# Optimization experiments

Hardware: AMD Instinct MI355X
Metric: run time of the kernel (lower is better)

## Reference

```python
import jax, jax.numpy as jnp
import numpy as np

B, H, W, P, KS = 4, 512, 512, 40000, 7
PAD = KS // 2
N = B * P
DIM, DEPTH, HID = 128, 2, 512


def _build_sparse_map():
    rng = np.random.default_rng(0)
    grid = np.full((B, H + 2 * PAD, W + 2 * PAD), N, dtype=np.int64)  # N = missing
    coords = np.empty((N, 3), np.int64)
    for b in range(B):
        flat = rng.choice(H * W, P, replace=False)
        xs, ys = flat // W, flat % W
        idx = np.arange(b * P, (b + 1) * P)
        grid[b, xs + PAD, ys + PAD] = idx
        coords[idx, 0], coords[idx, 1], coords[idx, 2] = b, xs, ys
    nbr = np.empty((N, KS * KS), np.int64)
    k = 0
    for dx in range(-PAD, PAD + 1):
        for dy in range(-PAD, PAD + 1):
            nbr[:, k] = grid[coords[:, 0], coords[:, 1] + PAD + dx, coords[:, 2] + PAD + dy]
            k += 1
    return nbr


def setup_inputs() -> dict:
    key = jax.random.key(0)
    ks = jax.random.split(key, 12)
    s = 0.02
    inp = {
        "feats": jax.random.normal(ks[0], (N, DIM), jnp.float32),
        "w_dw": jax.random.normal(ks[1], (DEPTH, KS * KS, DIM), jnp.float32) * s,
        "b_dw": jax.random.normal(ks[2], (DEPTH, DIM), jnp.float32) * s,
        "ln_g": jnp.ones((DEPTH, DIM), jnp.float32),
        "ln_b": jnp.zeros((DEPTH, DIM), jnp.float32),
        "w1": jax.random.normal(ks[3], (DEPTH, DIM, HID), jnp.float32) * s,
        "b1": jax.random.normal(ks[4], (DEPTH, HID), jnp.float32) * s,
        "grn_g": jax.random.normal(ks[5], (DEPTH, HID), jnp.float32) * s,
        "grn_b": jax.random.normal(ks[6], (DEPTH, HID), jnp.float32) * s,
        "w2": jax.random.normal(ks[7], (DEPTH, HID, DIM), jnp.float32) * s,
        "b2": jax.random.normal(ks[8], (DEPTH, DIM), jnp.float32) * s,
        "nbr_idx": jnp.asarray(_build_sparse_map()),
    }
    return inp


def _dwconv(x, w, b, nbr_t):
    # x: [N,C]; w: [K,C] per-offset per-channel; nbr_t: [K,N] (index N => missing)
    xp = jnp.concatenate([x, jnp.zeros((1, x.shape[1]), x.dtype)], axis=0)

    def step(acc, wn):
        wk, nk = wn
        return acc + xp[nk] * wk, None

    acc, _ = jax.lax.scan(step, jnp.zeros_like(x), (w, nbr_t))
    return acc + b


def _layernorm(x, g, b, eps=1e-6):
    mu = jnp.mean(x, axis=-1, keepdims=True)
    var = jnp.mean(jnp.square(x - mu), axis=-1, keepdims=True)
    return (x - mu) * jax.lax.rsqrt(var + eps) * g + b


def _grn(x, g, b):
    # global response norm over ALL points (dim 0), per channel (sparse ConvNeXtV2)
    gx = jnp.sqrt(jnp.sum(jnp.square(x), axis=0, keepdims=True))  # [1,C]
    nx = gx / (jnp.mean(gx, axis=-1, keepdims=True) + 1e-6)
    return g * (x * nx) + b + x


def reference(feats, w_dw, b_dw, ln_g, ln_b, w1, b1, grn_g, grn_b, w2, b2, nbr_idx):
    x = feats
    nbr_t = nbr_idx.T  # [K,N]
    for i in range(DEPTH):
        y = _dwconv(x, w_dw[i], b_dw[i], nbr_t)
        y = _layernorm(y, ln_g[i], ln_b[i])
        y = y @ w1[i] + b1[i]
        y = jax.nn.gelu(y, approximate=False)
        y = _grn(y, grn_g[i], grn_b[i])
        y = y @ w2[i] + b2[i]
        x = x + y  # drop_path = identity at eval
    return x
```

## Files before the change

### kernel.cpp

```cpp
#include <hip/hip_runtime.h>
#include <hip/hip_bf16.h>

#define NPTS   160000
#define DIM    128
#define HID    512
#define KK2    49
#define DEPTH  2

typedef __attribute__((ext_vector_type(8))) short bf16x8;
typedef __attribute__((ext_vector_type(4))) float f32x4;

static __device__ __forceinline__ ushort f2bf(float f) {
    unsigned u = __float_as_uint(f);
    return (ushort)((u + 0x7fffu + ((u >> 16) & 1u)) >> 16);
}
static __device__ __forceinline__ float bf2f(ushort h) {
    return __uint_as_float(((unsigned)h) << 16);
}
static __device__ __forceinline__ float lo16(unsigned u) { return __uint_as_float(u << 16); }
static __device__ __forceinline__ float hi16(unsigned u) { return __uint_as_float(u & 0xffff0000u); }

static __device__ __forceinline__ void cp16(const void* g, void* l) {
    __builtin_amdgcn_global_load_lds(
        (const __attribute__((address_space(1))) unsigned int*)g,
        (__attribute__((address_space(3))) unsigned int*)l,
        16, 0, 0);
}

static __device__ __forceinline__ float gelu_f(float v) {
    float x  = v * 0.70710678118654752f;
    float ax = fabsf(x);
    float t  = __builtin_amdgcn_rcpf(1.0f + 0.3275911f * ax);
    float p  = t * (0.254829592f + t * (-0.284496736f +
               t * (1.421413741f + t * (-1.453152027f + t * 1.061405429f))));
    float e  = __expf(-ax * ax);
    float er = copysignf(1.0f - p * e, x);
    return 0.5f * v * (1.0f + er);
}

__global__ __launch_bounds__(256) void cast_bf16_kernel(
    const float* __restrict__ x, ushort* __restrict__ o)
{
    int i = blockIdx.x * 256 + threadIdx.x;
    float4 v = ((const float4*)x)[i];
    ushort4 r;
    r.x = f2bf(v.x); r.y = f2bf(v.y); r.z = f2bf(v.z); r.w = f2bf(v.w);
    ((ushort4*)o)[i] = r;
}

__global__ void w1t_kernel(const float* __restrict__ w1, ushort* __restrict__ w1sw,
                           float* __restrict__ ssq) {
    int n = blockIdx.x;
    int k = threadIdx.x;
    int c = k >> 3, jj = k & 7;
    int dst = ((n >> 7) << 14) + ((n & 127) << 7) + ((c ^ (n & 15)) << 3) + jj;
    w1sw[dst] = f2bf(w1[k * 512 + n]);
    if (n < 4) ssq[n * 128 + k] = 0.f;
}

__global__ __launch_bounds__(256) void compact2_kernel(
    const int* __restrict__ nbr, int* __restrict__ wl, int* __restrict__ cnts)
{
    const int tid = threadIdx.x, lane = tid & 63, wv = tid >> 6;
    const int n = blockIdx.x * 4 + wv;
    int idx = (lane < KK2) ? nbr[(size_t)n * KK2 + lane] : NPTS;
    bool valid = idx < NPTS;
    unsigned long long mask = __ballot(valid);
    int cnt = __popcll(mask);
    int pos = __popcll(mask & ((1ull << lane) - 1ull));
    int* row = wl + (size_t)n * 64;
    if (lane >= cnt) row[lane] = 49;
    if (valid) row[pos] = (idx << 8) | lane;
    if (lane == 0) cnts[n] = cnt;
}

__global__ __launch_bounds__(1024, 8) void dwln5_kernel(
    const ushort* __restrict__ X,
    const int*    __restrict__ wl,
    const int*    __restrict__ cnts,
    const float*  __restrict__ wdw,
    const float*  __restrict__ bdw,
    const float*  __restrict__ lng,
    const float*  __restrict__ lnb,
    ushort*       __restrict__ y1)
{
    __shared__ __align__(16) float wsm[16 * 404];
    __shared__ int wle[64 * 68];
    const int tid = threadIdx.x;
    #pragma unroll
    for (int i0 = 0; i0 < 2048; i0 += 1024) {
        int i = i0 + tid;
        if (i < 1568) {
            int tap = i >> 5, rem = i & 31, cg = rem >> 1, q = rem & 1;
            ((float4*)wsm)[cg * 101 + tap * 2 + q] = ((const float4*)wdw)[i];
        }
    }
    if (tid < 32) {
        float4 z = {0.f, 0.f, 0.f, 0.f};
        int cg = tid >> 1, q = tid & 1;
        ((float4*)wsm)[cg * 101 + 98 + q] = z;
    }
    {
        const int* src = wl + (size_t)blockIdx.x * 4096;
        #pragma unroll
        for (int m = 0; m < 4; ++m) {
            int idx = tid + (m << 10);
            wle[(idx >> 6) * 68 + (idx & 63)] = src[idx];
        }
    }
    __syncthreads();

    const int lane = tid & 63, wv = tid >> 6;
    const int g = lane >> 4, cg = lane & 15;
    const int li = (wv << 2) + g;
    const int n = blockIdx.x * 64 + li;

    int myc = cnts[n];
    int rmax = max(myc, __shfl_xor(myc, 16));
    rmax = max(rmax, __shfl_xor(rmax, 32));

    const int* ep = wle + li * 68;
    const float* wcg = wsm + cg * 404;
    const char* Xb = (const char*)X + (cg << 4);

    float a[8] = {0.f, 0.f, 0.f, 0.f, 0.f, 0.f, 0.f, 0.f};

    int e0 = ep[0], e1 = ep[1], e2 = ep[2];
    uint4 x0 = *(const uint4*)(Xb + (e0 & ~255));
    uint4 x1 = *(const uint4*)(Xb + (e1 & ~255));
    uint4 x2 = *(const uint4*)(Xb + (e2 & ~255));

    for (int r = 0; r < rmax; ++r) {
        int e3 = ep[r + 3];
        uint4 x3 = *(const uint4*)(Xb + (e3 & ~255));
        const float* wp = wcg + (e0 & 255) * 8;
        float4 wa = *(const float4*)wp;
        float4 wb = *(const float4*)(wp + 4);
        a[0] += lo16(x0.x) * wa.x;  a[1] += hi16(x0.x) * wa.y;
        a[2] += lo16(x0.y) * wa.z;  a[3] += hi16(x0.y) * wa.w;
        a[4] += lo16(x0.z) * wb.x;  a[5] += hi16(x0.z) * wb.y;
        a[6] += lo16(x0.w) * wb.z;  a[7] += hi16(x0.w) * wb.w;
        e0 = e1; e1 = e2; e2 = e3;
        x0 = x1; x1 = x2; x2 = x3;
    }

    const float4 bda = ((const float4*)bdw)[cg * 2];
    const float4 bdb = ((const float4*)bdw)[cg * 2 + 1];
    a[0] += bda.x; a[1] += bda.y; a[2] += bda.z; a[3] += bda.w;
    a[4] += bdb.x; a[5] += bdb.y; a[6] += bdb.z; a[7] += bdb.w;

    float s1 = 0.f, s2 = 0.f;
    #pragma unroll
    for (int j = 0; j < 8; ++j) { s1 += a[j]; s2 += a[j] * a[j]; }
    #pragma unroll
    for (int m = 1; m < 16; m <<= 1) {
        s1 += __shfl_xor(s1, m);
        s2 += __shfl_xor(s2, m);
    }
    const float mu  = s1 * (1.f / 128.f);
    const float var = s2 * (1.f / 128.f) - mu * mu;
    const float rs  = rsqrtf(var + 1e-6f);

    const float4 ga = ((const float4*)lng)[cg * 2];
    const float4 gb = ((const float4*)lng)[cg * 2 + 1];
    const float4 ba = ((const float4*)lnb)[cg * 2];
    const float4 bb = ((const float4*)lnb)[cg * 2 + 1];
    uint4 r;
    r.x = (unsigned)f2bf((a[0] - mu) * rs * ga.x + ba.x)
        | ((unsigned)f2bf((a[1] - mu) * rs * ga.y + ba.y) << 16);
    r.y = (unsigned)f2bf((a[2] - mu) * rs * ga.z + ba.z)
        | ((unsigned)f2bf((a[3] - mu) * rs * ga.w + ba.w) << 16);
    r.z = (unsigned)f2bf((a[4] - mu) * rs * gb.x + bb.x)
        | ((unsigned)f2bf((a[5] - mu) * rs * gb.y + bb.y) << 16);
    r.w = (unsigned)f2bf((a[6] - mu) * rs * gb.z + bb.z)
        | ((unsigned)f2bf((a[7] - mu) * rs * gb.w + bb.w) << 16);
    ((uint4*)(y1 + (size_t)n * DIM))[cg] = r;
}

__global__ __launch_bounds__(256) void gemm1_kernel(
    const ushort* __restrict__ y1,
    const ushort* __restrict__ w1sw,
    const float*  __restrict__ b1,
    ushort*       __restrict__ y2,
    float*        __restrict__ ssq)
{
    __shared__ __align__(16) ushort sB[128 * 128];
    __shared__ float sred[HID];
    const int tid = threadIdx.x;
    const int lane = tid & 63, wv = tid >> 6;
    const int lr = lane & 15, q = lane >> 4;
    const int m0 = blockIdx.x << 7;
    const int mw = m0 + (wv << 5);

    #pragma unroll
    for (int i = tid; i < HID; i += 256) sred[i] = 0.f;

    bf16x8 af[2][4];
    {
        const ushort* a0 = y1 + (size_t)(mw + lr) * DIM + (q << 3);
        #pragma unroll
        for (int rt = 0; rt < 2; ++rt)
            #pragma unroll
            for (int ks = 0; ks < 4; ++ks)
                af[rt][ks] = *(const bf16x8*)(a0 + rt * 16 * DIM + ks * 32);
    }

    #pragma unroll 1
    for (int nt = 0; nt < 4; ++nt) {
        {
            const char* gsrc = (const char*)w1sw + (nt << 15) + (wv << 13) + (lane << 4);
            char* lb = (char*)sB + (wv << 13);
            #pragma unroll
            for (int j = 0; j < 8; ++j)
                cp16(gsrc + (j << 10), lb + (j << 10));
        }
        float b1v[8];
        #pragma unroll
        for (int ct = 0; ct < 8; ++ct) b1v[ct] = b1[(nt << 7) + (ct << 4) + lr];
        __syncthreads();

        f32x4 acc[2][8];
        #pragma unroll
        for (int ct = 0; ct < 8; ++ct) { f32x4 z = {0.f,0.f,0.f,0.f}; acc[0][ct] = z; acc[1][ct] = z; }

        #pragma unroll
        for (int ct = 0; ct < 8; ++ct)
            #pragma unroll
            for (int ks = 0; ks < 4; ++ks) {
                const int cidx = ((((ks << 2) + q) ^ lr) << 3);
                bf16x8 bfv = *(const bf16x8*)(sB + ((ct << 4) + lr) * 128 + cidx);
                acc[0][ct] = __builtin_amdgcn_mfma_f32_16x16x32_bf16(af[0][ks], bfv, acc[0][ct], 0, 0, 0);
                acc[1][ct] = __builtin_amdgcn_mfma_f32_16x16x32_bf16(af[1][ks], bfv, acc[1][ct], 0, 0, 0);
            }

        #pragma unroll
        for (int ct = 0; ct < 8; ++ct) {
            const int col = (nt << 7) + (ct << 4) + lr;
            float ss = 0.f;
            #pragma unroll
            for (int rt = 0; rt < 2; ++rt) {
                #pragma unroll
                for (int r = 0; r < 4; ++r) {
                    float g = gelu_f(acc[rt][ct][r] + b1v[ct]);
                    y2[(size_t)(mw + rt * 16 + (q << 2) + r) * HID + col] = f2bf(g);
                    ss += g * g;
                }
            }
            ss += __shfl_xor(ss, 16);
            ss += __shfl_xor(ss, 32);
            if (q == 0) atomicAdd(&sred[col], ss);
        }
        __syncthreads();
    }

    #pragma unroll
    for (int i = tid; i < HID; i += 256) atomicAdd(&ssq[i], sred[i]);
}

__global__ void grn_prep_kernel(const float* __restrict__ ssq,
                                const float* __restrict__ grn_g,
                                float* __restrict__ s)
{
    __shared__ float red[9];
    const int tid = threadIdx.x;
    const float gx = sqrtf(ssq[tid]);
    float v = gx;
    #pragma unroll
    for (int m = 1; m < 64; m <<= 1) v += __shfl_xor(v, m);
    if ((tid & 63) == 0) red[tid >> 6] = v;
    __syncthreads();
    if (tid == 0) {
        float t = 0.f;
        for (int i = 0; i < 8; ++i) t += red[i];
        red[8] = t;
    }
    __syncthreads();
    const float mean = red[8] * (1.f / 512.f);
    s[tid] = grn_g[tid] * (gx / (mean + 1e-6f)) + 1.0f;
}

__global__ __launch_bounds__(256) void prep_w2_kernel(
    const float* __restrict__ s,
    const float* __restrict__ w2,
    const float* __restrict__ grn_b,
    const float* __restrict__ b2,
    ushort*      __restrict__ w2sw,
    float*       __restrict__ bvec)
{
    __shared__ float r4[4];
    const int j = blockIdx.x;
    const int tid = threadIdx.x;
    float part = 0.f;
    for (int k = tid; k < HID; k += 256) {
        float wv2 = w2[k * 128 + j];
        int kk = k >> 7, c = (k >> 3) & 15, jj = k & 7;
        w2sw[(kk << 14) + (j << 7) + ((c ^ (j & 15)) << 3) + jj] = f2bf(s[k] * wv2);
        part += grn_b[k] * wv2;
    }
    #pragma unroll
    for (int m = 1; m < 64; m <<= 1) part += __shfl_xor(part, m);
    if ((tid & 63) == 0) r4[tid >> 6] = part;
    __syncthreads();
    if (tid == 0)
        bvec[j] = r4[0] + r4[1] + r4[2] + r4[3] + b2[j];
}

__global__ __launch_bounds__(256) void gemm2_kernel(
    const ushort* __restrict__ y2,
    const ushort* __restrict__ w2sw,
    const float*  __restrict__ bvec,
    const ushort* __restrict__ resid,
    float*        __restrict__ outf,
    ushort*       __restrict__ xbfout)
{
    __shared__ __align__(16) ushort sB[128 * 128];
    const int tid = threadIdx.x;
    const int lane = tid & 63, wv = tid >> 6;
    const int lr = lane & 15, q = lane >> 4;
    const int m0 = blockIdx.x << 7;
    const int mw = m0 + (wv << 5);

    f32x4 acc[2][8];
    #pragma unroll
    for (int ct = 0; ct < 8; ++ct) { f32x4 z = {0.f,0.f,0.f,0.f}; acc[0][ct] = z; acc[1][ct] = z; }

    const ushort* abase = y2 + (size_t)(mw + lr) * HID + (q << 3);

    #pragma unroll 1
    for (int kk = 0; kk < 4; ++kk) {
        bf16x8 af[2][4];
        #pragma unroll
        for (int rt = 0; rt < 2; ++rt)
            #pragma unroll
            for (int ks = 0; ks < 4; ++ks)
                af[rt][ks] = *(const bf16x8*)(abase + rt * 16 * HID + (kk << 7) + ks * 32);

        {
            const char* gsrc = (const char*)w2sw + (kk << 15) + (wv << 13) + (lane << 4);
            char* lb = (char*)sB + (wv << 13);
            #pragma unroll
            for (int j = 0; j < 8; ++j)
                cp16(gsrc + (j << 10), lb + (j << 10));
        }
        __syncthreads();

        #pragma unroll
        for (int ct = 0; ct < 8; ++ct)
            #pragma unroll
            for (int ks = 0; ks < 4; ++ks) {
                const int cidx = ((((ks << 2) + q) ^ lr) << 3);
                bf16x8 bfv = *(const bf16x8*)(sB + ((ct << 4) + lr) * 128 + cidx);
                acc[0][ct] = __builtin_amdgcn_mfma_f32_16x16x32_bf16(af[0][ks], bfv, acc[0][ct], 0, 0, 0);
                acc[1][ct] = __builtin_amdgcn_mfma_f32_16x16x32_bf16(af[1][ks], bfv, acc[1][ct], 0, 0, 0);
            }
        __syncthreads();
    }

    float bv[8];
    #pragma unroll
    for (int ct = 0; ct < 8; ++ct) bv[ct] = bvec[(ct << 4) + lr];

    #pragma unroll
    for (int rt = 0; rt < 2; ++rt)
        #pragma unroll
        for (int r = 0; r < 4; ++r) {
            const int m = mw + (rt << 4) + (q << 2) + r;
            const size_t base = (size_t)m * DIM;
            #pragma unroll
            for (int ct = 0; ct < 8; ++ct) {
                const int j = (ct << 4) + lr;
                float v = acc[rt][ct][r] + bv[ct] + bf2f(resid[base + j]);
                if (outf)   outf[base + j] = v;
                if (xbfout) xbfout[base + j] = f2bf(v);
            }
        }
}

extern "C" void kernel_launch(void* const* d_in, const int* in_sizes, int n_in,
                              void* d_out, int out_size, void* d_ws, size_t ws_size,
                              hipStream_t stream)
{
    const float* feats = (const float*)d_in[0];
    const float* w_dw  = (const float*)d_in[1];
    const float* b_dw  = (const float*)d_in[2];
    const float* ln_g  = (const float*)d_in[3];
    const float* ln_b  = (const float*)d_in[4];
    const float* w1    = (const float*)d_in[5];
    const float* b1    = (const float*)d_in[6];
    const float* grn_g = (const float*)d_in[7];
    const float* grn_b = (const float*)d_in[8];
    const float* w2    = (const float*)d_in[9];
    const float* b2    = (const float*)d_in[10];
    const int*   nbr   = (const int*)d_in[11];

    char* ws = (char*)d_ws;
    size_t o = 0;
    ushort* y2    = (ushort*)(ws + o); o += (size_t)NPTS * HID * 2;
    ushort* y1    = (ushort*)(ws + o); o += (size_t)NPTS * DIM * 2;
    ushort* xbf   = (ushort*)(ws + o); o += (size_t)NPTS * DIM * 2;
    int*    wl    = (int*)   (ws + o); o += ((size_t)NPTS * 64 + 64) * 4;
    int*    cnts  = (int*)   (ws + o); o += (size_t)NPTS * 4;
    ushort* w1sw  = (ushort*)(ws + o); o += (size_t)HID * DIM * 2;
    ushort* w2sw  = (ushort*)(ws + o); o += (size_t)HID * DIM * 2;
    float*  sbuf  = (float*) (ws + o); o += 2048;
    float*  ssq   = (float*) (ws + o); o += 2048;
    float*  bvec  = (float*) (ws + o); o += 512;

    cast_bf16_kernel<<<NPTS * DIM / 4 / 256, 256, 0, stream>>>(feats, xbf);
    compact2_kernel<<<NPTS / 4, 256, 0, stream>>>(nbr, wl, cnts);

    for (int l = 0; l < DEPTH; ++l) {
        const float* wdw_l = w_dw  + (size_t)l * KK2 * DIM;
        const float* bdw_l = b_dw  + (size_t)l * DIM;
        const float* lng_l = ln_g  + (size_t)l * DIM;
        const float* lnb_l = ln_b  + (size_t)l * DIM;
        const float* w1_l  = w1    + (size_t)l * DIM * HID;
        const float* b1_l  = b1    + (size_t)l * HID;
        const float* gg_l  = grn_g + (size_t)l * HID;
        const float* gb_l  = grn_b + (size_t)l * HID;
        const float* w2_l  = w2    + (size_t)l * HID * DIM;
        const float* b2_l  = b2    + (size_t)l * DIM;

        w1t_kernel<<<512, 128, 0, stream>>>(w1_l, w1sw, ssq);
        dwln5_kernel<<<NPTS / 64, 1024, 0, stream>>>(
            xbf, wl, cnts, wdw_l, bdw_l, lng_l, lnb_l, y1);
        gemm1_kernel<<<NPTS / 128, 256, 0, stream>>>(y1, w1sw, b1_l, y2, ssq);
        grn_prep_kernel<<<1, 512, 0, stream>>>(ssq, gg_l, sbuf);
        prep_w2_kernel<<<128, 256, 0, stream>>>(sbuf, w2_l, gb_l, b2_l, w2sw, bvec);
        if (l == 0) {
            gemm2_kernel<<<NPTS / 128, 256, 0, stream>>>(
                y2, w2sw, bvec, xbf, nullptr, xbf);
        } else {
            gemm2_kernel<<<NPTS / 128, 256, 0, stream>>>(
                y2, w2sw, bvec, xbf, (float*)d_out, nullptr);
        }
    }
}
```

Before: 697.5 us.

## Make GEMM kernels persistent with full weight matrix resident in LDS

Both GEMM kernels now launch 256 blocks of 1024 threads. Each block loads the entire 128x512 bf16 weight matrix (128KB) into LDS once, then each wave grid-strides over 16-row tiles. The intent is to stop reloading weights per 128-row tile and to remove the per-k-chunk syncs. In exchange each wave now works on 16 rows instead of 32, so there is less A-fragment reuse per B read from LDS. Occupancy is limited to one block per CU because of the large LDS footprint.

```diff
diff --git a/kernel.cpp b/kernel.cpp
--- a/kernel.cpp
+++ b/kernel.cpp
@@ -177,84 +177,65 @@
     ((uint4*)(y1 + (size_t)n * DIM))[cg] = r;
 }
 
-__global__ __launch_bounds__(256) void gemm1_kernel(
+__global__ __launch_bounds__(1024) void gemm1_kernel(
     const ushort* __restrict__ y1,
     const ushort* __restrict__ w1sw,
     const float*  __restrict__ b1,
     ushort*       __restrict__ y2,
     float*        __restrict__ ssq)
 {
-    __shared__ __align__(16) ushort sB[128 * 128];
+    __shared__ __align__(16) ushort sB[65536];
     __shared__ float sred[HID];
     const int tid = threadIdx.x;
     const int lane = tid & 63, wv = tid >> 6;
     const int lr = lane & 15, q = lane >> 4;
-    const int m0 = blockIdx.x << 7;
-    const int mw = m0 + (wv << 5);
-
-    #pragma unroll
-    for (int i = tid; i < HID; i += 256) sred[i] = 0.f;
-
-    bf16x8 af[2][4];
+
+    if (tid < HID) sred[tid] = 0.f;
     {
-        const ushort* a0 = y1 + (size_t)(mw + lr) * DIM + (q << 3);
-        #pragma unroll
-        for (int rt = 0; rt < 2; ++rt)
-            #pragma unroll
-            for (int ks = 0; ks < 4; ++ks)
-                af[rt][ks] = *(const bf16x8*)(a0 + rt * 16 * DIM + ks * 32);
-    }
-
-    #pragma unroll 1
-    for (int nt = 0; nt < 4; ++nt) {
-        {
-            const char* gsrc = (const char*)w1sw + (nt << 15) + (wv << 13) + (lane << 4);
-            char* lb = (char*)sB + (wv << 13);
-            #pragma unroll
-            for (int j = 0; j < 8; ++j)
-                cp16(gsrc + (j << 10), lb + (j << 10));
-        }
-        float b1v[8];
-        #pragma unroll
-        for (int ct = 0; ct < 8; ++ct) b1v[ct] = b1[(nt << 7) + (ct << 4) + lr];
-        __syncthreads();
-
-        f32x4 acc[2][8];
-        #pragma unroll
-        for (int ct = 0; ct < 8; ++ct) { f32x4 z = {0.f,0.f,0.f,0.f}; acc[0][ct] = z; acc[1][ct] = z; }
-
-        #pragma unroll
-        for (int ct = 0; ct < 8; ++ct)
+        const char* g = (const char*)w1sw + (wv << 13) + (lane << 4);
+        char* l = (char*)sB + (wv << 13);
+        #pragma unroll
+        for (int j = 0; j < 8; ++j)
+            cp16(g + (j << 10), l + (j << 10));
+    }
+    __syncthreads();
+
+    const int gw = blockIdx.x * 16 + wv;
+    for (int t = gw; t < NPTS / 16; t += 4096) {
+        const int m0 = t << 4;
+        bf16x8 af[4];
+        const ushort* a0 = y1 + (size_t)(m0 + lr) * DIM + (q << 3);
+        #pragma unroll
+        for (int ks = 0; ks < 4; ++ks)
+            af[ks] = *(const bf16x8*)(a0 + ks * 32);
+
+        #pragma unroll 1
+        for (int ct = 0; ct < 32; ++ct) {
+            const ushort* sb = sB + ((ct >> 3) << 14) + (((ct & 7) << 4) + lr) * 128;
+            f32x4 acc = {0.f, 0.f, 0.f, 0.f};
             #pragma unroll
             for (int ks = 0; ks < 4; ++ks) {
                 const int cidx = ((((ks << 2) + q) ^ lr) << 3);
-                bf16x8 bfv = *(const bf16x8*)(sB + ((ct << 4) + lr) * 128 + cidx);
-                acc[0][ct] = __builtin_amdgcn_mfma_f32_16x16x32_bf16(af[0][ks], bfv, acc[0][ct], 0, 0, 0);
-                acc[1][ct] = __builtin_amdgcn_mfma_f32_16x16x32_bf16(af[1][ks], bfv, acc[1][ct], 0, 0, 0);
+                bf16x8 bfv = *(const bf16x8*)(sb + cidx);
+                acc = __builtin_amdgcn_mfma_f32_16x16x32_bf16(af[ks], bfv, acc, 0, 0, 0);
             }
-
-        #pragma unroll
-        for (int ct = 0; ct < 8; ++ct) {
-            const int col = (nt << 7) + (ct << 4) + lr;
+            const int col = (ct << 4) + lr;
+            const float bv = b1[col];
             float ss = 0.f;
             #pragma unroll
-            for (int rt = 0; rt < 2; ++rt) {
-                #pragma unroll
-                for (int r = 0; r < 4; ++r) {
-                    float g = gelu_f(acc[rt][ct][r] + b1v[ct]);
-                    y2[(size_t)(mw + rt * 16 + (q << 2) + r) * HID + col] = f2bf(g);
-                    ss += g * g;
-                }
+            for (int r = 0; r < 4; ++r) {
+                float g = gelu_f(acc[r] + bv);
+                y2[(size_t)(m0 + (q << 2) + r) * HID + col] = f2bf(g);
+                ss += g * g;
             }
             ss += __shfl_xor(ss, 16);
             ss += __shfl_xor(ss, 32);
             if (q == 0) atomicAdd(&sred[col], ss);
         }
-        __syncthreads();
-    }
-
-    #pragma unroll
-    for (int i = tid; i < HID; i += 256) atomicAdd(&ssq[i], sred[i]);
+    }
+
+    __syncthreads();
+    if (tid < HID) atomicAdd(&ssq[tid], sred[tid]);
 }
 
 __global__ void grn_prep_kernel(const float* __restrict__ ssq,
@@ -305,7 +286,7 @@
         bvec[j] = r4[0] + r4[1] + r4[2] + r4[3] + b2[j];
 }
 
-__global__ __launch_bounds__(256) void gemm2_kernel(
+__global__ __launch_bounds__(1024) void gemm2_kernel(
     const ushort* __restrict__ y2,
     const ushort* __restrict__ w2sw,
     const float*  __restrict__ bvec,
@@ -313,67 +294,63 @@
     float*        __restrict__ outf,
     ushort*       __restrict__ xbfout)
 {
-    __shared__ __align__(16) ushort sB[128 * 128];
+    __shared__ __align__(16) ushort sB[65536];
     const int tid = threadIdx.x;
     const int lane = tid & 63, wv = tid >> 6;
     const int lr = lane & 15, q = lane >> 4;
-    const int m0 = blockIdx.x << 7;
-    const int mw = m0 + (wv << 5);
-
-    f32x4 acc[2][8];
-    #pragma unroll
-    for (int ct = 0; ct < 8; ++ct) { f32x4 z = {0.f,0.f,0.f,0.f}; acc[0][ct] = z; acc[1][ct] = z; }
-
-    const ushort* abase = y2 + (size_t)(mw + lr) * HID + (q << 3);
-
-    #pragma unroll 1
-    for (int kk = 0; kk < 4; ++kk) {
-        bf16x8 af[2][4];
-        #pragma unroll
-        for (int rt = 0; rt < 2; ++rt)
+
+    {
+        const char* g = (const char*)w2sw + (wv << 13) + (lane << 4);
+        char* l = (char*)sB + (wv << 13);
+        #pragma unroll
+        for (int j = 0; j < 8; ++j)
+            cp16(g + (j << 10), l + (j << 10));
+    }
+    __syncthreads();
+
+    float bv[8];
+    #pragma unroll
+    for (int ct = 0; ct < 8; ++ct) bv[ct] = bvec[(ct << 4) + lr];
+
+    const int gw = blockIdx.x * 16 + wv;
+    for (int t = gw; t < NPTS / 16; t += 4096) {
+        const int m0 = t << 4;
+        f32x4 acc[8];
+        #pragma unroll
+        for (int ct = 0; ct < 8; ++ct) { f32x4 z = {0.f,0.f,0.f,0.f}; acc[ct] = z; }
+
+        const ushort* abase = y2 + (size_t)(m0 + lr) * HID + (q << 3);
+        #pragma unroll
+        for (int kc = 0; kc < 4; ++kc) {
+            bf16x8 af[4];
             #pragma unroll
             for (int ks = 0; ks < 4; ++ks)
-                af[rt][ks] = *(const bf16x8*)(abase + rt * 16 * HID + (kk << 7) + ks * 32);
-
-        {
-            const char* gsrc = (const char*)w2sw + (kk << 15) + (wv << 13) + (lane << 4);
-            char* lb = (char*)sB + (wv << 13);
+                af[ks] = *(const bf16x8*)(abase + (kc << 7) + ks * 32);
             #pragma unroll
-            for (int j = 0; j < 8; ++j)
-                cp16(gsrc + (j << 10), lb + (j << 10));
-        }
-        __syncthreads();
-
-        #pragma unroll
-        for (int ct = 0; ct < 8; ++ct)
-            #pragma unroll
-            for (int ks = 0; ks < 4; ++ks) {
-                const int cidx = ((((ks << 2) + q) ^ lr) << 3);
-                bf16x8 bfv = *(const bf16x8*)(sB + ((ct << 4) + lr) * 128 + cidx);
-                acc[0][ct] = __builtin_amdgcn_mfma_f32_16x16x32_bf16(af[0][ks], bfv, acc[0][ct], 0, 0, 0);
-                acc[1][ct] = __builtin_amdgcn_mfma_f32_16x16x32_bf16(af[1][ks], bfv, acc[1][ct], 0, 0, 0);
+            for (int ct = 0; ct < 8; ++ct) {
+                const ushort* sb = sB + (kc << 14) + (((ct << 4) + lr) * 128);
+                #pragma unroll
+                for (int ks = 0; ks < 4; ++ks) {
+                    const int cidx = ((((ks << 2) + q) ^ lr) << 3);
+                    bf16x8 bfv = *(const bf16x8*)(sb + cidx);
+                    acc[ct] = __builtin_amdgcn_mfma_f32_16x16x32_bf16(af[ks], bfv, acc[ct], 0, 0, 0);
+                }
             }
-        __syncthreads();
-    }
-
-    float bv[8];
-    #pragma unroll
-    for (int ct = 0; ct < 8; ++ct) bv[ct] = bvec[(ct << 4) + lr];
-
-    #pragma unroll
-    for (int rt = 0; rt < 2; ++rt)
+        }
+
         #pragma unroll
         for (int r = 0; r < 4; ++r) {
-            const int m = mw + (rt << 4) + (q << 2) + r;
+            const int m = m0 + (q << 2) + r;
             const size_t base = (size_t)m * DIM;
             #pragma unroll
             for (int ct = 0; ct < 8; ++ct) {
                 const int j = (ct << 4) + lr;
-                float v = acc[rt][ct][r] + bv[ct] + bf2f(resid[base + j]);
+                float v = acc[ct][r] + bv[ct] + bf2f(resid[base + j]);
                 if (outf)   outf[base + j] = v;
                 if (xbfout) xbfout[base + j] = f2bf(v);
             }
         }
+    }
 }
 
 extern "C" void kernel_launch(void* const* d_in, const int* in_sizes, int n_in,
@@ -424,14 +401,14 @@
         w1t_kernel<<<512, 128, 0, stream>>>(w1_l, w1sw, ssq);
         dwln5_kernel<<<NPTS / 64, 1024, 0, stream>>>(
             xbf, wl, cnts, wdw_l, bdw_l, lng_l, lnb_l, y1);
-        gemm1_kernel<<<NPTS / 128, 256, 0, stream>>>(y1, w1sw, b1_l, y2, ssq);
+        gemm1_kernel<<<256, 1024, 0, stream>>>(y1, w1sw, b1_l, y2, ssq);
         grn_prep_kernel<<<1, 512, 0, stream>>>(ssq, gg_l, sbuf);
         prep_w2_kernel<<<128, 256, 0, stream>>>(sbuf, w2_l, gb_l, b2_l, w2sw, bvec);
         if (l == 0) {
-            gemm2_kernel<<<NPTS / 128, 256, 0, stream>>>(
+            gemm2_kernel<<<256, 1024, 0, stream>>>(
                 y2, w2sw, bvec, xbf, nullptr, xbf);
         } else {
-            gemm2_kernel<<<NPTS / 128, 256, 0, stream>>>(
+            gemm2_kernel<<<256, 1024, 0, stream>>>(
                 y2, w2sw, bvec, xbf, (float*)d_out, nullptr);
         }
     }
```

Measured after the change: 1.491 ms. +113.7%, slower.
